# Optimization experiments

Hardware: AMD Instinct MI355X
Metric: run time of the kernel (lower is better)

The kernel has to match this reference:

```python
import jax, jax.numpy as jnp
import numpy as np

EPS = 1e-5
K = 3          # deform conv kernel size
N = K * K      # 9 sampling points per output pixel


def conv2d(x, w, b=None):
    # x [B,C,H,W], w [O,I,kh,kw], stride 1, SAME padding (== torch padding=k//2)
    y = jax.lax.conv_general_dilated(x, w, (1, 1), 'SAME',
                                     dimension_numbers=('NCHW', 'OIHW', 'NCHW'))
    if b is not None:
        y = y + b[None, :, None, None]
    return y


def bilinear_sample(img, y, x):
    # img [B,C,H,W]; y,x [B,N,H,W] float sampling coordinates; zero padding outside.
    B, C, H, W = img.shape
    y0 = jnp.floor(y); x0 = jnp.floor(x)
    wy1 = y - y0; wy0 = 1.0 - wy1
    wx1 = x - x0; wx0 = 1.0 - wx1
    img_flat = img.reshape(B, C, H * W)

    def gather(yy, xx):
        valid = (yy >= 0) & (yy <= H - 1) & (xx >= 0) & (xx <= W - 1)
        yc = jnp.clip(yy, 0, H - 1).astype(jnp.int32)
        xc = jnp.clip(xx, 0, W - 1).astype(jnp.int32)
        idx = (yc * W + xc).reshape(B, -1)                      # [B, N*H*W]
        v = jax.vmap(lambda im, ix: im[:, ix])(img_flat, idx)   # [B, C, N*H*W]
        v = v.reshape(B, C, N, H, W)
        return v * valid[:, None].astype(img.dtype)

    v00 = gather(y0,     x0)
    v01 = gather(y0,     x0 + 1)
    v10 = gather(y0 + 1, x0)
    v11 = gather(y0 + 1, x0 + 1)
    wy0 = wy0[:, None]; wy1 = wy1[:, None]
    wx0 = wx0[:, None]; wx1 = wx1[:, None]
    return wy0 * (wx0 * v00 + wx1 * v01) + wy1 * (wx0 * v10 + wx1 * v11)


def deform_conv(x, w_off, b_off, w):
    # DeformConv2d(k=3, pad=1, stride=1, bias=False): offsets predicted by a 3x3 conv,
    # per-pixel bilinear sampling at p0 + pn + offset, then 3x3 weighted sum.
    B, C, H, W = x.shape
    off = conv2d(x, w_off, b_off)               # [B, 2N, H, W]
    dy, dx = off[:, :N], off[:, N:]
    ky, kx = jnp.meshgrid(jnp.arange(K) - 1, jnp.arange(K) - 1, indexing='ij')
    ky = ky.reshape(N).astype(x.dtype)
    kx = kx.reshape(N).astype(x.dtype)
    ii = jnp.arange(H, dtype=x.dtype)[None, None, :, None]
    jj = jnp.arange(W, dtype=x.dtype)[None, None, None, :]
    ysamp = ii + ky[None, :, None, None] + dy   # [B,N,H,W]
    xsamp = jj + kx[None, :, None, None] + dx
    s = bilinear_sample(x, ysamp, xsamp)        # [B,C,N,H,W]
    Cout = w.shape[0]
    return jnp.einsum('bcnhw,ocn->bohw', s, w.reshape(Cout, C, N))


def batchnorm_relu(x, gamma, beta):
    # train-mode BatchNorm2d (batch statistics, biased variance) + ReLU
    m = x.mean(axis=(0, 2, 3), keepdims=True)
    v = x.var(axis=(0, 2, 3), keepdims=True)
    xn = (x - m) * jax.lax.rsqrt(v + EPS)
    return jax.nn.relu(xn * gamma[None, :, None, None] + beta[None, :, None, None])


def maxpool2(x):
    return jax.lax.reduce_window(x, -jnp.inf, jax.lax.max,
                                 (1, 1, 2, 2), (1, 1, 2, 2), 'VALID')


def setup_inputs() -> dict:
    key = jax.random.key(0)
    ks = jax.random.split(key, 16)
    B, Cin, Cout, H, W = 4, 32, 64, 256, 256
    Hp, Wp = H // 2, W // 2
    f = jax.random.normal
    inp = {
        'x':  f(ks[0], (B, Cin, H, W), jnp.float32),
        'h0': f(ks[1], (B, Cout, Hp, Wp), jnp.float32),
        'c0': f(ks[2], (B, Cout, Hp, Wp), jnp.float32),
        # deform conv 1: Cin -> Cout
        'w_off1': f(ks[3], (2 * N, Cin, K, K), jnp.float32) * 0.01,
        'b_off1': jnp.zeros((2 * N,), jnp.float32),
        'w1': f(ks[4], (Cout, Cin, K, K), jnp.float32) * 0.05,
        'g1': jnp.ones((Cout,), jnp.float32),
        'be1': jnp.zeros((Cout,), jnp.float32),
        # deform conv 2: Cout -> Cout
        'w_off2': f(ks[5], (2 * N, Cout, K, K), jnp.float32) * 0.01,
        'b_off2': jnp.zeros((2 * N,), jnp.float32),
        'w2': f(ks[6], (Cout, Cout, K, K), jnp.float32) * 0.05,
        'g2': jnp.ones((Cout,), jnp.float32),
        'be2': jnp.zeros((Cout,), jnp.float32),
        # ConvLSTM gates: conv(cat(x, h)) -> 4*hidden channels
        'w_gates': f(ks[7], (4 * Cout, 2 * Cout, K, K), jnp.float32) * 0.05,
        'b_gates': jnp.zeros((4 * Cout,), jnp.float32),
    }
    return inp


def reference(x, h0, c0, w_off1, b_off1, w1, g1, be1,
              w_off2, b_off2, w2, g2, be2, w_gates, b_gates):
    # maxpool_conv = MaxPool2d(2) -> DoubleDConv (deform conv + BN + ReLU, twice)
    x = maxpool2(x)
    x = batchnorm_relu(deform_conv(x, w_off1, b_off1, w1), g1, be1)
    x = batchnorm_relu(deform_conv(x, w_off2, b_off2, w2), g2, be2)
    # ConvLSTM cell
    gates = conv2d(jnp.concatenate([x, h0], axis=1), w_gates, b_gates)
    i, f, o, g = jnp.split(gates, 4, axis=1)
    c = jax.nn.sigmoid(f) * c0 + jax.nn.sigmoid(i) * jnp.tanh(g)
    h = jax.nn.sigmoid(o) * jnp.tanh(c)
    # module returns (x, state) with x == hidden, state == (hidden, cell)
    return h, c
```

## Files before the change

### kernel.cpp

```cpp
#include <hip/hip_runtime.h>
#include <hip/hip_fp16.h>
#include <math.h>

#define P 128
#define NP (P*P)
#define BATCH 4

typedef __attribute__((ext_vector_type(8))) short bf16x8;
typedef __attribute__((ext_vector_type(8))) _Float16 h16x8;
typedef __attribute__((ext_vector_type(4))) float f32x4;

__device__ __forceinline__ float sigmoidf_(float x){ return 1.f/(1.f+__expf(-x)); }
__device__ __forceinline__ float tanhf_(float x){
  float ax = fabsf(x);
  float e = __expf(2.f*ax);
  float t = 1.f - 2.f/(e + 1.f);
  return copysignf(t, x);
}
__device__ __forceinline__ short f2bf(float f){
  unsigned u = __builtin_bit_cast(unsigned, f);
  u = (u + 0x7FFFu + ((u>>16)&1u)) >> 16;
  return (short)u;
}
__device__ __forceinline__ short f2h(float f){
  return (short)__half_as_short(__float2half(f));
}

__global__ void maxpool_cl_k(const float* __restrict__ x, float* __restrict__ xp){
  int idx = blockIdx.x*256 + threadIdx.x;
  if (idx >= BATCH*NP) return;
  int wp = idx & (P-1); int t = idx >> 7; int hp = t & (P-1); int b = t >> 7;
  const float* src = x + ((size_t)b*32*65536) + (size_t)(hp*2)*256 + wp*2;
  float m[32];
  #pragma unroll
  for (int c = 0; c < 32; c++){
    const float* s = src + (size_t)c*65536;
    m[c] = fmaxf(fmaxf(s[0], s[1]), fmaxf(s[256], s[257]));
  }
  float* dst = xp + (size_t)idx*32;
  #pragma unroll
  for (int q = 0; q < 8; q++) *(float4*)(dst + q*4) = *(float4*)(m + q*4);
}

__global__ void wprep_all_k(const float* __restrict__ wg, const float* __restrict__ w1,
                            const float* __restrict__ w2, const float* __restrict__ wo1,
                            const float* __restrict__ wo2,
                            short* __restrict__ wA, short* __restrict__ wd1T,
                            short* __restrict__ wd2T, short* __restrict__ woT1,
                            short* __restrict__ woT2){
  int idx = blockIdx.x*256 + threadIdx.x;
  if (idx < 294912){
    int s = idx & 7; int l = (idx>>3) & 63; int mb = (idx>>9) & 15;
    int cb = (idx>>13) & 3; int tap = idx >> 15;
    int ln = l & 15, kg = l >> 4;
    int r = mb*16 + ln; int ch = r >> 2, gate = r & 3;
    int cin = cb*32 + kg*8 + s;
    wA[idx] = f2bf(wg[((size_t)(gate*64 + ch)*128 + cin)*9 + tap]);
    return;
  }
  idx -= 294912;
  if (idx < 18432){
    int s = idx & 7; int l = (idx>>3) & 63; int mb = (idx>>9) & 3; int tap = idx >> 11;
    int ln = l & 15, kg = l >> 4;
    int o = mb*16 + ln; int cin = kg*8 + s;
    wd1T[idx] = f2h(w1[((size_t)(o*32 + cin))*9 + tap]);
    return;
  }
  idx -= 18432;
  if (idx < 36864){
    int s = idx & 7; int l = (idx>>3) & 63; int mb = (idx>>9) & 3;
    int cb = (idx>>11) & 1; int tap = idx >> 12;
    int ln = l & 15, kg = l >> 4;
    int o = mb*16 + ln; int cin = cb*32 + kg*8 + s;
    wd2T[idx] = f2h(w2[((size_t)(o*64 + cin))*9 + tap]);
    return;
  }
  idx -= 36864;
  if (idx < 9216){
    int s = idx & 7; int l = (idx>>3) & 63; int mb = (idx>>9) & 1; int tap = idx >> 10;
    int ln = l & 15, kg = l >> 4;
    int o = mb*16 + ln; int cin = kg*8 + s;
    woT1[idx] = (o < 18) ? f2h(wo1[((size_t)(o*32 + cin))*9 + tap]) : (short)0;
    return;
  }
  idx -= 9216;
  if (idx < 18432){
    int s = idx & 7; int l = (idx>>3) & 63; int mb = (idx>>9) & 1;
    int cb = (idx>>10) & 1; int tap = idx >> 11;
    int ln = l & 15, kg = l >> 4;
    int o = mb*16 + ln; int cin = cb*32 + kg*8 + s;
    woT2[idx] = (o < 18) ? f2h(wo2[((size_t)(o*64 + cin))*9 + tap]) : (short)0;
  }
}

template<int CIN, bool BNIN>
__global__ __launch_bounds__(256) void deform_fused_k(
    const float* __restrict__ incl, const float* __restrict__ bstats,
    const float* __restrict__ b_off,
    const short* __restrict__ woT, const short* __restrict__ wdT,
    float* __restrict__ outcl, float* __restrict__ part){
  const int HS = 14, NHP = HS*HS;
  const int ROWB = CIN*2;
  const int CG = CIN/8, CGS = (CIN==64)?3:2;
  const int PM = (CIN==64)?7:3;
  const int NCB = CIN/32;
  __shared__ short xt[NHP*CIN];
  __shared__ float off_lds[64][20];
  __shared__ float red_s[4][64], red_q[4][64];
  int tid = threadIdx.x;
  int tile = blockIdx.x, b = blockIdx.y;
  int tx0 = (tile & 15)*8, ty0 = (tile >> 4)*8;
  const float* inb = incl + (size_t)b*NP*CIN;
  for (int e = tid; e < NHP*CG; e += 256){
    int cg = e & (CG-1), p = e >> CGS;
    int hr = p/HS, wc = p - hr*HS;
    int gy = ty0 + hr - 3, gx = tx0 + wc - 3;
    union { short s[8]; __half2 h[4]; h16x8 v; } u;
    if (((unsigned)gy < P) && ((unsigned)gx < P)){
      const float* src = inb + ((size_t)gy*P + gx)*CIN + cg*8;
      float4 a = *(const float4*)src, bb = *(const float4*)(src+4);
      if (BNIN){
        int c = cg*8;
        a.x = fmaxf(a.x*bstats[c+0]+bstats[64+c+0], 0.f);
        a.y = fmaxf(a.y*bstats[c+1]+bstats[64+c+1], 0.f);
        a.z = fmaxf(a.z*bstats[c+2]+bstats[64+c+2], 0.f);
        a.w = fmaxf(a.w*bstats[c+3]+bstats[64+c+3], 0.f);
        bb.x = fmaxf(bb.x*bstats[c+4]+bstats[64+c+4], 0.f);
        bb.y = fmaxf(bb.y*bstats[c+5]+bstats[64+c+5], 0.f);
        bb.z = fmaxf(bb.z*bstats[c+6]+bstats[64+c+6], 0.f);
        bb.w = fmaxf(bb.w*bstats[c+7]+bstats[64+c+7], 0.f);
      }
      u.h[0] = __float22half2_rn(float2{a.x, a.y});
      u.h[1] = __float22half2_rn(float2{a.z, a.w});
      u.h[2] = __float22half2_rn(float2{bb.x, bb.y});
      u.h[3] = __float22half2_rn(float2{bb.z, bb.w});
    } else {
      #pragma unroll
      for (int j = 0; j < 8; j++) u.s[j] = 0;
    }
    *(h16x8*)((char*)xt + p*ROWB + ((cg*16) ^ ((p & PM)<<4))) = u.v;
  }
  __syncthreads();

  int lane = tid & 63, wid = tid >> 6;
  int kg = lane >> 4, ln = lane & 15;
  int py = ty0 + wid*2 + (ln>>3), pxg = tx0 + (ln&7);
  int pl = wid*16 + ln;

  {
    f32x4 acc_o[2];
    acc_o[0] = (f32x4){0.f,0.f,0.f,0.f};
    acc_o[1] = (f32x4){0.f,0.f,0.f,0.f};
    #pragma unroll
    for (int tap = 0; tap < 9; tap++){
      int ky = tap/3, kx = tap - (tap/3)*3;
      int lr = wid*2 + (ln>>3) + ky + 2;
      int lc = (ln&7) + kx + 2;
      int p = lr*HS + lc;
      #pragma unroll
      for (int cb = 0; cb < NCB; cb++){
        h16x8 bfv = *(const h16x8*)((const char*)xt + p*ROWB + (((cb*64) + kg*16) ^ ((p & PM)<<4)));
        h16x8 af0 = *(const h16x8*)(const void*)(woT + ((size_t)((tap*NCB + cb)*2 + 0)*512 + lane*8));
        h16x8 af1 = *(const h16x8*)(const void*)(woT + ((size_t)((tap*NCB + cb)*2 + 1)*512 + lane*8));
        acc_o[0] = __builtin_amdgcn_mfma_f32_16x16x32_f16(af0, bfv, acc_o[0], 0, 0, 0);
        acc_o[1] = __builtin_amdgcn_mfma_f32_16x16x32_f16(af1, bfv, acc_o[1], 0, 0, 0);
      }
    }
    #pragma unroll
    for (int mf = 0; mf < 2; mf++){
      #pragma unroll
      for (int j = 0; j < 4; j++){
        int o = mf*16 + kg*4 + j;
        if (o < 18) off_lds[pl][o] = acc_o[mf][j] + b_off[o];
      }
    }
  }
  __syncthreads();

  f32x4 acc[4];
  #pragma unroll
  for (int mf = 0; mf < 4; mf++) acc[mf] = (f32x4){0.f,0.f,0.f,0.f};

  for (int tap = 0; tap < 9; tap++){
    float dy = off_lds[pl][tap], dx = off_lds[pl][9+tap];
    float ys = (float)(py + tap/3 - 1) + dy;
    float xs = (float)(pxg + tap%3 - 1) + dx;
    float y0f = floorf(ys), x0f = floorf(xs);
    float wy1 = ys - y0f, wx1 = xs - x0f;
    float wy0 = 1.f - wy1, wx0 = 1.f - wx1;
    int y0 = (int)y0f, x0 = (int)x0f;
    bool v0y = ((unsigned)y0 < P), v1y = ((unsigned)(y0+1) < P);
    bool v0x = ((unsigned)x0 < P), v1x = ((unsigned)(x0+1) < P);
    float w00 = (v0y && v0x) ? wy0*wx0 : 0.f;
    float w01 = (v0y && v1x) ? wy0*wx1 : 0.f;
    float w10 = (v1y && v0x) ? wy1*wx0 : 0.f;
    float w11 = (v1y && v1x) ? wy1*wx1 : 0.f;
    __half2 w00h = __float2half2_rn(w00);
    __half2 w01h = __float2half2_rn(w01);
    __half2 w10h = __float2half2_rn(w10);
    __half2 w11h = __float2half2_rn(w11);
    int ly0 = min(max(y0 - ty0 + 3, 0), HS-1);
    int ly1 = min(max(y0 + 1 - ty0 + 3, 0), HS-1);
    int lx0 = min(max(x0 - tx0 + 3, 0), HS-1);
    int lx1 = min(max(x0 + 1 - tx0 + 3, 0), HS-1);
    int p00 = ly0*HS + lx0, p01 = ly0*HS + lx1;
    int p10 = ly1*HS + lx0, p11 = ly1*HS + lx1;
    #pragma unroll
    for (int cb = 0; cb < NCB; cb++){
      int ko = (cb*32 + kg*8)*2;
      union { __half2 h[4]; h16x8 v; } c00, c01, c10, c11, bu;
      c00.v = *(const h16x8*)((const char*)xt + p00*ROWB + (ko ^ ((p00 & PM)<<4)));
      c01.v = *(const h16x8*)((const char*)xt + p01*ROWB + (ko ^ ((p01 & PM)<<4)));
      c10.v = *(const h16x8*)((const char*)xt + p10*ROWB + (ko ^ ((p10 & PM)<<4)));
      c11.v = *(const h16x8*)((const char*)xt + p11*ROWB + (ko ^ ((p11 & PM)<<4)));
      #pragma unroll
      for (int j = 0; j < 4; j++){
        bu.h[j] = __hfma2(c00.h[j], w00h,
                  __hfma2(c01.h[j], w01h,
                  __hfma2(c10.h[j], w10h,
                  __hmul2(c11.h[j], w11h))));
      }
      #pragma unroll
      for (int mf = 0; mf < 4; mf++){
        h16x8 af = *(const h16x8*)(const void*)(wdT + ((size_t)((tap*NCB + cb)*4 + mf)*512 + lane*8));
        acc[mf] = __builtin_amdgcn_mfma_f32_16x16x32_f16(af, bu.v, acc[mf], 0, 0, 0);
      }
    }
  }
  #pragma unroll
  for (int mf = 0; mf < 4; mf++){
    float* dst = outcl + ((size_t)b*NP + (size_t)py*P + pxg)*64 + mf*16 + kg*4;
    *(f32x4*)dst = acc[mf];
  }

  #pragma unroll
  for (int mf = 0; mf < 4; mf++){
    #pragma unroll
    for (int j = 0; j < 4; j++){
      float s = acc[mf][j], q = s*s;
      #pragma unroll
      for (int o = 1; o < 16; o <<= 1){
        s += __shfl_xor(s, o);
        q += __shfl_xor(q, o);
      }
      if (ln == 0){
        int ch = mf*16 + kg*4 + j;
        red_s[wid][ch] = s;
        red_q[wid][ch] = q;
      }
    }
  }
  __syncthreads();
  int blk = b*256 + tile;
  if (tid < 128){
    int ch = tid & 63;
    float v = (tid < 64)
      ? (red_s[0][ch]+red_s[1][ch]+red_s[2][ch]+red_s[3][ch])
      : (red_q[0][ch]+red_q[1][ch]+red_q[2][ch]+red_q[3][ch]);
    part[(size_t)tid*1024 + blk] = v;
  }
}

__global__ void bnfinal2_k(const float* __restrict__ part, const float* __restrict__ g,
                           const float* __restrict__ be, float* __restrict__ stats){
  int ch = blockIdx.x;
  int tid = threadIdx.x;
  float S = 0.f, Q = 0.f;
  for (int i = tid; i < 1024; i += 256){
    S += part[(size_t)ch*1024 + i];
    Q += part[(size_t)(64+ch)*1024 + i];
  }
  __shared__ float rs[256], rq[256];
  rs[tid] = S; rq[tid] = Q;
  __syncthreads();
  for (int o = 128; o > 0; o >>= 1){
    if (tid < o){ rs[tid] += rs[tid+o]; rq[tid] += rq[tid+o]; }
    __syncthreads();
  }
  if (tid == 0){
    const float inv = 1.f/(float)(BATCH*NP);
    float mean = rs[0]*inv;
    float var = rq[0]*inv - mean*mean;
    float scale = rsqrtf(var + 1e-5f)*g[ch];
    stats[ch] = scale;
    stats[64+ch] = be[ch] - mean*scale;
  }
}

__global__ void h2cl_k(const float* __restrict__ h0, short* __restrict__ hcl){
  __shared__ float t[64][65];
  int b = blockIdx.y;
  int p0 = blockIdx.x*64;
  int pl = threadIdx.x & 63;
  int cq = threadIdx.x >> 6;
  const float* src = h0 + (size_t)b*64*NP + p0 + pl;
  #pragma unroll
  for (int i = 0; i < 16; i++)
    t[cq*16+i][pl] = src[(size_t)(cq*16+i)*NP];
  __syncthreads();
  int p = threadIdx.x >> 2, q = threadIdx.x & 3;
  short* dst = hcl + ((size_t)(b*NP + p0 + p))*64 + q*16;
  union { short s[8]; bf16x8 v; } o0, o1;
  #pragma unroll
  for (int i = 0; i < 8; i++){ o0.s[i] = f2bf(t[q*16+i][p]); o1.s[i] = f2bf(t[q*16+8+i][p]); }
  *(bf16x8*)dst = o0.v;
  *(bf16x8*)(dst+8) = o1.v;
}

__global__ __launch_bounds__(512, 4) void gates_mfma_k(
    const float* __restrict__ y2, const float* __restrict__ stats,
    const short* __restrict__ hcl, const float* __restrict__ c0,
    const short* __restrict__ wA, const float* __restrict__ bg,
    float* __restrict__ outh, float* __restrict__ outc){
  extern __shared__ short lds[];
  short* bs = lds;
  short* abuf = lds + 180*128;
  int tid = threadIdx.x;
  int tile = blockIdx.x, b = blockIdx.y;
  int tx0 = (tile & 7)*16, ty0 = (tile >> 3)*8;
  int lane = tid & 63, wid = tid >> 6;

  for (int e = tid; e < 180*16; e += 512){
    int cg = e & 15, p = e >> 4;
    int hr = p/18, wc = p - hr*18;
    int gy = ty0 + hr - 1, gx = tx0 + wc - 1;
    union { short s[8]; bf16x8 v; } u;
    if (((unsigned)gy < P) && ((unsigned)gx < P)){
      if (cg < 8){
        const float* src = y2 + ((size_t)(b*NP) + (size_t)gy*P + gx)*64 + cg*8;
        float4 a = *(const float4*)src, b4 = *(const float4*)(src+4);
        int c = cg*8;
        u.s[0] = f2bf(fmaxf(a.x*stats[c+0]+stats[64+c+0], 0.f));
        u.s[1] = f2bf(fmaxf(a.y*stats[c+1]+stats[64+c+1], 0.f));
        u.s[2] = f2bf(fmaxf(a.z*stats[c+2]+stats[64+c+2], 0.f));
        u.s[3] = f2bf(fmaxf(a.w*stats[c+3]+stats[64+c+3], 0.f));
        u.s[4] = f2bf(fmaxf(b4.x*stats[c+4]+stats[64+c+4], 0.f));
        u.s[5] = f2bf(fmaxf(b4.y*stats[c+5]+stats[64+c+5], 0.f));
        u.s[6] = f2bf(fmaxf(b4.z*stats[c+6]+stats[64+c+6], 0.f));
        u.s[7] = f2bf(fmaxf(b4.w*stats[c+7]+stats[64+c+7], 0.f));
      } else {
        u.v = *(const bf16x8*)(hcl + ((size_t)(b*NP) + (size_t)gy*P + gx)*64 + (cg-8)*8);
      }
    } else {
      #pragma unroll
      for (int j = 0; j < 8; j++) u.s[j] = 0;
    }
    *(bf16x8*)((char*)bs + p*256 + ((cg*16) ^ ((p&7)<<4))) = u.v;
  }

  auto stageA = [&](int c, int bi){
    const short* g = wA + (size_t)c*8192;
    short* l = abuf + bi*8192;
    #pragma unroll
    for (int i = 0; i < 2; i++){
      int unit = wid*2 + i;
      __builtin_amdgcn_global_load_lds(
          (const __attribute__((address_space(1))) unsigned int*)(g + (size_t)(unit*64 + lane)*8),
          (__attribute__((address_space(3))) unsigned int*)(l + (size_t)unit*512),
          16, 0, 0);
    }
  };

  stageA(0, 0);
  stageA(1, 1);
  __syncthreads();

  int kg = lane >> 4, ln = lane & 15;
  int ct = wid >> 1, nh = wid & 1;
  f32x4 acc[4][4];
  #pragma unroll
  for (int mf = 0; mf < 4; mf++)
    #pragma unroll
    for (int rr = 0; rr < 4; rr++) acc[mf][rr] = (f32x4){0.f,0.f,0.f,0.f};

  for (int c = 0; c < 36; c++){
    int cur = c & 1;
    int tap = c >> 2, cb = c & 3;
    int ky = tap/3, kx = tap - ky*3;
    const short* al = abuf + cur*8192;
    bf16x8 af[4], bf[4];
    #pragma unroll
    for (int mf = 0; mf < 4; mf++)
      af[mf] = *(const bf16x8*)(al + (size_t)(ct*4 + mf)*512 + lane*8);
    #pragma unroll
    for (int rr = 0; rr < 4; rr++){
      int p = (nh*4 + rr + ky)*18 + ln + kx;
      bf[rr] = *(const bf16x8*)((const char*)bs + p*256 + (((cb*64) + kg*16) ^ ((p&7)<<4)));
    }
    asm volatile("s_waitcnt lgkmcnt(0)" ::: "memory");
    __builtin_amdgcn_sched_barrier(0);
    __builtin_amdgcn_s_barrier();
    __builtin_amdgcn_sched_barrier(0);
    if (c + 2 < 36) stageA(c + 2, cur);
    #pragma unroll
    for (int rr = 0; rr < 4; rr++)
      #pragma unroll
      for (int mf = 0; mf < 4; mf++)
        acc[mf][rr] = __builtin_amdgcn_mfma_f32_16x16x32_bf16(af[mf], bf[rr], acc[mf][rr], 0, 0, 0);
    if (c + 2 < 36){
      asm volatile("s_waitcnt vmcnt(2)" ::: "memory");
    } else {
      asm volatile("s_waitcnt vmcnt(0)" ::: "memory");
    }
    __builtin_amdgcn_sched_barrier(0);
    __builtin_amdgcn_s_barrier();
    __builtin_amdgcn_sched_barrier(0);
  }

  #pragma unroll
  for (int mf = 0; mf < 4; mf++){
    int ch = ct*16 + mf*4 + kg;
    float bi = bg[ch], bff = bg[64+ch], bo = bg[128+ch], bgv = bg[192+ch];
    #pragma unroll
    for (int rr = 0; rr < 4; rr++){
      int py = ty0 + nh*4 + rr, px = tx0 + ln;
      size_t pidx = ((size_t)(b*64 + ch))*NP + (size_t)py*P + px;
      f32x4 a = acc[mf][rr];
      float cv = sigmoidf_(a[1]+bff)*c0[pidx] + sigmoidf_(a[0]+bi)*tanhf_(a[3]+bgv);
      float hv = sigmoidf_(a[2]+bo)*tanhf_(cv);
      outh[pidx] = hv;
      outc[pidx] = cv;
    }
  }
}

extern "C" void kernel_launch(void* const* d_in, const int* in_sizes, int n_in,
                              void* d_out, int out_size, void* d_ws, size_t ws_size,
                              hipStream_t stream) {
  const float* x      = (const float*)d_in[0];
  const float* h0     = (const float*)d_in[1];
  const float* c0     = (const float*)d_in[2];
  const float* w_off1 = (const float*)d_in[3];
  const float* b_off1 = (const float*)d_in[4];
  const float* w1     = (const float*)d_in[5];
  const float* g1     = (const float*)d_in[6];
  const float* be1    = (const float*)d_in[7];
  const float* w_off2 = (const float*)d_in[8];
  const float* b_off2 = (const float*)d_in[9];
  const float* w2     = (const float*)d_in[10];
  const float* g2     = (const float*)d_in[11];
  const float* be2    = (const float*)d_in[12];
  const float* wg     = (const float*)d_in[13];
  const float* bg     = (const float*)d_in[14];

  float* ws     = (float*)d_ws;
  float* xpcl   = ws;
  short* hcl    = (short*)ws;
  float* y1     = ws + 2097152;
  float* y2     = ws + 6291456;
  float* part   = ws + 10485760;
  float* stats1 = ws + 10616832;
  float* stats2 = ws + 10616960;
  short* wA     = (short*)(ws + 10617088);
  short* wd1T   = wA + 294912;
  short* wd2T   = wd1T + 18432;
  short* woT1   = wd2T + 36864;
  short* woT2   = woT1 + 9216;

  (void)hipFuncSetAttribute((const void*)gates_mfma_k,
                            hipFuncAttributeMaxDynamicSharedMemorySize, 78848);

  maxpool_cl_k<<<dim3((BATCH*NP + 255)/256), dim3(256), 0, stream>>>(x, xpcl);
  wprep_all_k<<<dim3((377856 + 255)/256), dim3(256), 0, stream>>>(
      wg, w1, w2, w_off1, w_off2, wA, wd1T, wd2T, woT1, woT2);

  deform_fused_k<32,false><<<dim3(256, BATCH), dim3(256), 0, stream>>>(
      xpcl, stats1, b_off1, woT1, wd1T, y1, part);
  h2cl_k<<<dim3(NP/64, BATCH), dim3(256), 0, stream>>>(h0, hcl);
  bnfinal2_k<<<dim3(64), dim3(256), 0, stream>>>(part, g1, be1, stats1);

  deform_fused_k<64,true><<<dim3(256, BATCH), dim3(256), 0, stream>>>(
      y1, stats1, b_off2, woT2, wd2T, y2, part);
  bnfinal2_k<<<dim3(64), dim3(256), 0, stream>>>(part, g2, be2, stats2);

  float* outh = (float*)d_out;
  float* outc = outh + (size_t)BATCH*64*NP;
  gates_mfma_k<<<dim3(128, BATCH), dim3(512), 78848, stream>>>(
      y2, stats2, hcl, c0, wA, bg, outh, outc);
}
```

Baseline: 124.0 us.

## Merge small prep kernels and reuse B-fragment window across ky taps in gates GEMM

```diff
diff --git a/kernel.cpp b/kernel.cpp
--- a/kernel.cpp
+++ b/kernel.cpp
@@ -26,32 +26,35 @@
   return (short)__half_as_short(__float2half(f));
 }
 
-__global__ void maxpool_cl_k(const float* __restrict__ x, float* __restrict__ xp){
-  int idx = blockIdx.x*256 + threadIdx.x;
-  if (idx >= BATCH*NP) return;
-  int wp = idx & (P-1); int t = idx >> 7; int hp = t & (P-1); int b = t >> 7;
-  const float* src = x + ((size_t)b*32*65536) + (size_t)(hp*2)*256 + wp*2;
-  float m[32];
-  #pragma unroll
-  for (int c = 0; c < 32; c++){
-    const float* s = src + (size_t)c*65536;
-    m[c] = fmaxf(fmaxf(s[0], s[1]), fmaxf(s[256], s[257]));
-  }
-  float* dst = xp + (size_t)idx*32;
-  #pragma unroll
-  for (int q = 0; q < 8; q++) *(float4*)(dst + q*4) = *(float4*)(m + q*4);
-}
-
-__global__ void wprep_all_k(const float* __restrict__ wg, const float* __restrict__ w1,
-                            const float* __restrict__ w2, const float* __restrict__ wo1,
-                            const float* __restrict__ wo2,
-                            short* __restrict__ wA, short* __restrict__ wd1T,
-                            short* __restrict__ wd2T, short* __restrict__ woT1,
-                            short* __restrict__ woT2){
-  int idx = blockIdx.x*256 + threadIdx.x;
+__global__ void prep_k(const float* __restrict__ x, float* __restrict__ xp,
+                       const float* __restrict__ wg, const float* __restrict__ w1,
+                       const float* __restrict__ w2, const float* __restrict__ wo1,
+                       const float* __restrict__ wo2,
+                       short* __restrict__ wA, short* __restrict__ wd1T,
+                       short* __restrict__ wd2T, short* __restrict__ woT1,
+                       short* __restrict__ woT2){
+  int bx = blockIdx.x;
+  if (bx < 256){
+    int idx = bx*256 + threadIdx.x;
+    int wp = idx & (P-1); int t = idx >> 7; int hp = t & (P-1); int b = t >> 7;
+    const float* src = x + ((size_t)b*32*65536) + (size_t)(hp*2)*256 + wp*2;
+    float m[32];
+    #pragma unroll
+    for (int c = 0; c < 32; c++){
+      const float* s = src + (size_t)c*65536;
+      m[c] = fmaxf(fmaxf(s[0], s[1]), fmaxf(s[256], s[257]));
+    }
+    float* dst = xp + (size_t)idx*32;
+    #pragma unroll
+    for (int q = 0; q < 8; q++) *(float4*)(dst + q*4) = *(float4*)(m + q*4);
+    return;
+  }
+  int idx = (bx - 256)*256 + threadIdx.x;
   if (idx < 294912){
     int s = idx & 7; int l = (idx>>3) & 63; int mb = (idx>>9) & 15;
-    int cb = (idx>>13) & 3; int tap = idx >> 15;
+    int t = idx >> 13;
+    int ky = t % 3; int t2 = t / 3; int kx = t2 % 3; int cb = t2 / 3;
+    int tap = ky*3 + kx;
     int ln = l & 15, kg = l >> 4;
     int r = mb*16 + ln; int ch = r >> 2, gate = r & 3;
     int cin = cb*32 + kg*8 + s;
@@ -287,24 +290,55 @@
   }
 }
 
-__global__ void h2cl_k(const float* __restrict__ h0, short* __restrict__ hcl){
-  __shared__ float t[64][65];
-  int b = blockIdx.y;
-  int p0 = blockIdx.x*64;
-  int pl = threadIdx.x & 63;
-  int cq = threadIdx.x >> 6;
-  const float* src = h0 + (size_t)b*64*NP + p0 + pl;
-  #pragma unroll
-  for (int i = 0; i < 16; i++)
-    t[cq*16+i][pl] = src[(size_t)(cq*16+i)*NP];
-  __syncthreads();
-  int p = threadIdx.x >> 2, q = threadIdx.x & 3;
-  short* dst = hcl + ((size_t)(b*NP + p0 + p))*64 + q*16;
-  union { short s[8]; bf16x8 v; } o0, o1;
-  #pragma unroll
-  for (int i = 0; i < 8; i++){ o0.s[i] = f2bf(t[q*16+i][p]); o1.s[i] = f2bf(t[q*16+8+i][p]); }
-  *(bf16x8*)dst = o0.v;
-  *(bf16x8*)(dst+8) = o1.v;
+__global__ void aux1_k(const float* __restrict__ part, const float* __restrict__ g,
+                       const float* __restrict__ be, float* __restrict__ stats,
+                       const float* __restrict__ h0, short* __restrict__ hcl){
+  int bx = blockIdx.x;
+  int tid = threadIdx.x;
+  if (bx < 64){
+    int ch = bx;
+    float S = 0.f, Q = 0.f;
+    for (int i = tid; i < 1024; i += 256){
+      S += part[(size_t)ch*1024 + i];
+      Q += part[(size_t)(64+ch)*1024 + i];
+    }
+    __shared__ float rs[256], rq[256];
+    rs[tid] = S; rq[tid] = Q;
+    __syncthreads();
+    for (int o = 128; o > 0; o >>= 1){
+      if (tid < o){ rs[tid] += rs[tid+o]; rq[tid] += rq[tid+o]; }
+      __syncthreads();
+    }
+    if (tid == 0){
+      const float inv = 1.f/(float)(BATCH*NP);
+      float mean = rs[0]*inv;
+      float var = rq[0]*inv - mean*mean;
+      float scale = rsqrtf(var + 1e-5f)*g[ch];
+      stats[ch] = scale;
+      stats[64+ch] = be[ch] - mean*scale;
+    }
+    return;
+  }
+  {
+    __shared__ float t[64][65];
+    int blk = bx - 64;
+    int b = blk >> 8;
+    int p0 = (blk & 255)*64;
+    int pl = tid & 63;
+    int cq = tid >> 6;
+    const float* src = h0 + (size_t)b*64*NP + p0 + pl;
+    #pragma unroll
+    for (int i = 0; i < 16; i++)
+      t[cq*16+i][pl] = src[(size_t)(cq*16+i)*NP];
+    __syncthreads();
+    int p = tid >> 2, q = tid & 3;
+    short* dst = hcl + ((size_t)(b*NP + p0 + p))*64 + q*16;
+    union { short s[8]; bf16x8 v; } o0, o1;
+    #pragma unroll
+    for (int i = 0; i < 8; i++){ o0.s[i] = f2bf(t[q*16+i][p]); o1.s[i] = f2bf(t[q*16+8+i][p]); }
+    *(bf16x8*)dst = o0.v;
+    *(bf16x8*)(dst+8) = o1.v;
+  }
 }
 
 __global__ __launch_bounds__(512, 4) void gates_mfma_k(
@@ -373,38 +407,52 @@
     #pragma unroll
     for (int rr = 0; rr < 4; rr++) acc[mf][rr] = (f32x4){0.f,0.f,0.f,0.f};
 
-  for (int c = 0; c < 36; c++){
-    int cur = c & 1;
-    int tap = c >> 2, cb = c & 3;
-    int ky = tap/3, kx = tap - ky*3;
-    const short* al = abuf + cur*8192;
-    bf16x8 af[4], bf[4];
-    #pragma unroll
-    for (int mf = 0; mf < 4; mf++)
-      af[mf] = *(const bf16x8*)(al + (size_t)(ct*4 + mf)*512 + lane*8);
-    #pragma unroll
-    for (int rr = 0; rr < 4; rr++){
-      int p = (nh*4 + rr + ky)*18 + ln + kx;
-      bf[rr] = *(const bf16x8*)((const char*)bs + p*256 + (((cb*64) + kg*16) ^ ((p&7)<<4)));
-    }
-    asm volatile("s_waitcnt lgkmcnt(0)" ::: "memory");
-    __builtin_amdgcn_sched_barrier(0);
-    __builtin_amdgcn_s_barrier();
-    __builtin_amdgcn_sched_barrier(0);
-    if (c + 2 < 36) stageA(c + 2, cur);
-    #pragma unroll
-    for (int rr = 0; rr < 4; rr++)
-      #pragma unroll
-      for (int mf = 0; mf < 4; mf++)
-        acc[mf][rr] = __builtin_amdgcn_mfma_f32_16x16x32_bf16(af[mf], bf[rr], acc[mf][rr], 0, 0, 0);
-    if (c + 2 < 36){
-      asm volatile("s_waitcnt vmcnt(2)" ::: "memory");
-    } else {
-      asm volatile("s_waitcnt vmcnt(0)" ::: "memory");
-    }
-    __builtin_amdgcn_sched_barrier(0);
-    __builtin_amdgcn_s_barrier();
-    __builtin_amdgcn_sched_barrier(0);
+  bf16x8 bwin[6];
+  #pragma unroll
+  for (int cb = 0; cb < 4; cb++){
+    #pragma unroll
+    for (int kx = 0; kx < 3; kx++){
+      #pragma unroll
+      for (int ky = 0; ky < 3; ky++){
+        const int cc = (cb*3 + kx)*3 + ky;
+        const short* al = abuf + (cc & 1)*8192;
+        if (ky == 0){
+          #pragma unroll
+          for (int j = 0; j < 4; j++){
+            int p = (nh*4 + j)*18 + ln + kx;
+            bwin[j] = *(const bf16x8*)((const char*)bs + p*256 + (((cb*64) + kg*16) ^ ((p&7)<<4)));
+          }
+        } else {
+          const int j = ky + 3;
+          int p = (nh*4 + j)*18 + ln + kx;
+          bwin[j] = *(const bf16x8*)((const char*)bs + p*256 + (((cb*64) + kg*16) ^ ((p&7)<<4)));
+        }
+        bf16x8 af[4];
+        #pragma unroll
+        for (int mf = 0; mf < 4; mf++)
+          af[mf] = *(const bf16x8*)(al + (size_t)(ct*4 + mf)*512 + lane*8);
+        asm volatile("s_waitcnt lgkmcnt(0)" ::: "memory");
+        __builtin_amdgcn_sched_barrier(0);
+        __builtin_amdgcn_s_barrier();
+        __builtin_amdgcn_sched_barrier(0);
+        if (cc + 2 < 36) stageA(cc + 2, cc & 1);
+        __builtin_amdgcn_s_setprio(1);
+        #pragma unroll
+        for (int rr = 0; rr < 4; rr++)
+          #pragma unroll
+          for (int mf = 0; mf < 4; mf++)
+            acc[mf][rr] = __builtin_amdgcn_mfma_f32_16x16x32_bf16(af[mf], bwin[rr + ky], acc[mf][rr], 0, 0, 0);
+        __builtin_amdgcn_s_setprio(0);
+        if (cc + 2 < 36){
+          asm volatile("s_waitcnt vmcnt(2)" ::: "memory");
+        } else {
+          asm volatile("s_waitcnt vmcnt(0)" ::: "memory");
+        }
+        __builtin_amdgcn_sched_barrier(0);
+        __builtin_amdgcn_s_barrier();
+        __builtin_amdgcn_sched_barrier(0);
+      }
+    }
   }
 
   #pragma unroll
@@ -460,14 +508,12 @@
   (void)hipFuncSetAttribute((const void*)gates_mfma_k,
                             hipFuncAttributeMaxDynamicSharedMemorySize, 78848);
 
-  maxpool_cl_k<<<dim3((BATCH*NP + 255)/256), dim3(256), 0, stream>>>(x, xpcl);
-  wprep_all_k<<<dim3((377856 + 255)/256), dim3(256), 0, stream>>>(
-      wg, w1, w2, w_off1, w_off2, wA, wd1T, wd2T, woT1, woT2);
+  prep_k<<<dim3(256 + 1476), dim3(256), 0, stream>>>(
+      x, xpcl, wg, w1, w2, w_off1, w_off2, wA, wd1T, wd2T, woT1, woT2);
 
   deform_fused_k<32,false><<<dim3(256, BATCH), dim3(256), 0, stream>>>(
       xpcl, stats1, b_off1, woT1, wd1T, y1, part);
-  h2cl_k<<<dim3(NP/64, BATCH), dim3(256), 0, stream>>>(h0, hcl);
-  bnfinal2_k<<<dim3(64), dim3(256), 0, stream>>>(part, g1, be1, stats1);
+  aux1_k<<<dim3(64 + 1024), dim3(256), 0, stream>>>(part, g1, be1, stats1, h0, hcl);
 
   deform_fused_k<64,true><<<dim3(256, BATCH), dim3(256), 0, stream>>>(
       y1, stats1, b_off2, woT2, wd2T, y2, part);
```

Result: no change. 123.5 us (-0.4%).
